# Optimization experiments

Hardware: AMD Instinct MI355X
Metric: run time of the kernel (lower is better)

The kernel has to match this reference:

```python
import jax, jax.numpy as jnp
import numpy as np

MIN_SCALE = 1e-3
TEMPERATURE = 1.5


def setup_inputs() -> dict:
    key = jax.random.key(0)
    ks = jax.random.split(key, 9)
    B, S, D, R, C = 1024, 64, 512, 16, 1000
    s = 1.0 / np.sqrt(D)  # scale weights for numerical sanity
    return {
        "features": jax.random.normal(ks[0], (B, D), jnp.float32),
        "W_cov": jax.random.normal(ks[1], (D * R, D), jnp.float32) * s,
        "b_cov": jnp.zeros((D * R,), jnp.float32),
        "W_diag": jax.random.normal(ks[2], (D, D), jnp.float32) * s,
        "b_diag": jnp.zeros((D,), jnp.float32),
        "W_cls": jax.random.normal(ks[3], (C, D), jnp.float32) * s,
        "b_cls": jnp.zeros((C,), jnp.float32),
        "noise_diag": jax.random.normal(ks[4], (B, S, D), jnp.float32),
        "noise_lr": jax.random.normal(ks[5], (B, S, R), jnp.float32),
    }


def reference(features, W_cov, b_cov, W_diag, b_diag, W_cls, b_cls, noise_diag, noise_lr):
    B, D = features.shape
    R = noise_lr.shape[-1]
    # Linear(D -> D*R), reshape to (B, D, R) (row-major, matches torch .reshape)
    low_rank_cov = (features @ W_cov.T + b_cov).reshape(B, D, R)
    # diagonal std: softplus(Linear(D->D)) + min_scale
    diagonal_std = jax.nn.softplus(features @ W_diag.T + b_diag) + MIN_SCALE
    # samples: low-rank part + diagonal part, both (B, S, D)
    samples = (
        jnp.einsum("bdr,bsr->bsd", low_rank_cov, noise_lr)
        + diagonal_std[:, None, :] * noise_diag
    )
    pre_logits = features[:, None, :] + samples  # (B, S, D)
    logits = pre_logits @ W_cls.T + b_cls  # (B, S, C)
    return logits / TEMPERATURE
```

## Files before the change

### kernel.cpp

```cpp
#include <hip/hip_runtime.h>
#include <math.h>

typedef __attribute__((ext_vector_type(8))) short bf16x8;
typedef __attribute__((ext_vector_type(4))) float f32x4;
typedef __attribute__((ext_vector_type(4))) unsigned short u16x4;

__device__ inline unsigned short f2bf(float f) {
    union { float f; unsigned u; } v; v.f = f;
    unsigned r = v.u + 0x7FFFu + ((v.u >> 16) & 1u);
    return (unsigned short)(r >> 16);
}
__device__ inline float bf2f(unsigned short h) {
    union { unsigned u; float f; } v; v.u = ((unsigned)h) << 16;
    return v.f;
}

__device__ inline void load_lds16(const void* g, void* l) {
    __builtin_amdgcn_global_load_lds(
        (const __attribute__((address_space(1))) unsigned int*)g,
        (__attribute__((address_space(3))) unsigned int*)l,
        16, 0, 0);
}

__global__ __launch_bounds__(256) void convert_all(
    const float* __restrict__ sA, unsigned short* __restrict__ dA, long nA,
    const float* __restrict__ sB, unsigned short* __restrict__ dB, long nB,
    const float* __restrict__ sC, unsigned short* __restrict__ dC, long nC,
    const float* __restrict__ sD, unsigned short* __restrict__ dD, long nDs, long nDd)
{
    long i = ((long)blockIdx.x * 256 + threadIdx.x) * 4;
    const float* s; unsigned short* d; long nsrc;
    if (i < nA)              { s = sA + i; d = dA + i; nsrc = nA - i; }
    else if ((i -= nA) < nB) { s = sB + i; d = dB + i; nsrc = nB - i; }
    else if ((i -= nB) < nC) { s = sC + i; d = dC + i; nsrc = nC - i; }
    else if ((i -= nC) < nDd){ s = sD + i; d = dD + i; nsrc = nDs - i; }
    else return;
    float4 v = make_float4(0.f, 0.f, 0.f, 0.f);
    if (nsrc >= 4) v = *(const float4*)s;
    u16x4 o;
    o[0] = f2bf(v.x); o[1] = f2bf(v.y); o[2] = f2bf(v.z); o[3] = f2bf(v.w);
    *(u16x4*)d = o;
}

template <int MODE, bool SWZ>
__global__ __launch_bounds__(256) void gemm_bf16(
    const unsigned short* __restrict__ A, const unsigned short* __restrict__ Bm,
    const float* __restrict__ bias0, const float* __restrict__ bias1,
    void* __restrict__ out0v, void* __restrict__ out1v,
    int M, int Npad, int Nreal, int K, int nsplit)
{
    __shared__ __align__(16) unsigned short As[128 * 64];
    __shared__ __align__(16) unsigned short Bs[128 * 64];

    const int tid  = threadIdx.x;
    const int nblk = Npad >> 7;
    int mt, nt;
    if constexpr (SWZ) {
        const int per = (M >> 7) >> 3;
        const int x = blockIdx.x & 7;
        const int j = blockIdx.x >> 3;
        const int jm = j / nblk;
        mt = x * per + jm;
        nt = j - jm * nblk;
    } else {
        mt = blockIdx.x / nblk;
        nt = blockIdx.x - mt * nblk;
    }
    const int m0 = mt << 7;
    const int n0 = nt << 7;

    const int lane = tid & 63;
    const int wid  = tid >> 6;
    const int wm   = (wid & 1) << 6;
    const int wn   = (wid >> 1) << 6;
    const int quad = lane >> 4;
    const int l15  = lane & 15;
    const int l7   = l15 & 7;

    const int lrow = lane >> 3;
    const int lcol = ((lane & 7) ^ lrow) << 3;

    const unsigned short* Ab = A  + (size_t)(m0 + wid * 32 + lrow) * K + lcol;
    const unsigned short* Bb = Bm + (size_t)(n0 + wid * 32 + lrow) * K + lcol;
    unsigned short* AsW = &As[(wid * 32) * 64];
    unsigned short* BsW = &Bs[(wid * 32) * 64];

    f32x4 acc[4][4];
    #pragma unroll
    for (int i = 0; i < 4; ++i)
        #pragma unroll
        for (int j = 0; j < 4; ++j)
            acc[i][j] = f32x4{0.f, 0.f, 0.f, 0.f};

    for (int kt = 0; kt < K; kt += 64) {
        __syncthreads();
        #pragma unroll
        for (int i = 0; i < 4; ++i) {
            load_lds16(Ab + (size_t)(i * 8) * K + kt, AsW + i * 8 * 64);
            load_lds16(Bb + (size_t)(i * 8) * K + kt, BsW + i * 8 * 64);
        }
        __syncthreads();

        #pragma unroll
        for (int kk = 0; kk < 64; kk += 32) {
            const int kq = kk >> 3;
            bf16x8 af[4], bfv[4];
            #pragma unroll
            for (int mi = 0; mi < 4; ++mi)
                af[mi] = *(const bf16x8*)&As[(wm + mi * 16 + l15) * 64
                                             + (((kq + quad) ^ l7) << 3)];
            #pragma unroll
            for (int ni = 0; ni < 4; ++ni)
                bfv[ni] = *(const bf16x8*)&Bs[(wn + ni * 16 + l15) * 64
                                              + (((kq + quad) ^ l7) << 3)];
            #pragma unroll
            for (int mi = 0; mi < 4; ++mi)
                #pragma unroll
                for (int ni = 0; ni < 4; ++ni)
                    acc[mi][ni] = __builtin_amdgcn_mfma_f32_16x16x32_bf16(
                        bfv[ni], af[mi], acc[mi][ni], 0, 0, 0);
        }
    }

    if constexpr (MODE == 2) {
        float* o = (float*)out0v;
        #pragma unroll
        for (int ni = 0; ni < 4; ++ni) {
            const int nb = n0 + wn + ni * 16 + (quad << 2);
            if (nb >= Nreal) continue;
            const float4 bv = *(const float4*)&bias0[nb];
            #pragma unroll
            for (int mi = 0; mi < 4; ++mi) {
                const int m = m0 + wm + mi * 16 + l15;
                f32x4 v;
                v[0] = (acc[mi][ni][0] + bv.x) * (1.0f / 1.5f);
                v[1] = (acc[mi][ni][1] + bv.y) * (1.0f / 1.5f);
                v[2] = (acc[mi][ni][2] + bv.z) * (1.0f / 1.5f);
                v[3] = (acc[mi][ni][3] + bv.w) * (1.0f / 1.5f);
                *(f32x4*)&o[(size_t)m * Nreal + nb] = v;
            }
        }
    } else {
        if (n0 < nsplit) {
            unsigned short* o = (unsigned short*)out0v;
            #pragma unroll
            for (int ni = 0; ni < 4; ++ni) {
                const int nb = n0 + wn + ni * 16 + (quad << 2);
                const float4 bv = *(const float4*)&bias0[nb];
                #pragma unroll
                for (int mi = 0; mi < 4; ++mi) {
                    const int m = m0 + wm + mi * 16 + l15;
                    u16x4 ov;
                    ov[0] = f2bf(acc[mi][ni][0] + bv.x);
                    ov[1] = f2bf(acc[mi][ni][1] + bv.y);
                    ov[2] = f2bf(acc[mi][ni][2] + bv.z);
                    ov[3] = f2bf(acc[mi][ni][3] + bv.w);
                    *(u16x4*)&o[(size_t)m * nsplit + nb] = ov;
                }
            }
        } else {
            float* o = (float*)out1v;
            const int ld1 = Npad - nsplit;
            #pragma unroll
            for (int ni = 0; ni < 4; ++ni) {
                const int nb = n0 + wn + ni * 16 + (quad << 2) - nsplit;
                const float4 bv = *(const float4*)&bias1[nb];
                #pragma unroll
                for (int mi = 0; mi < 4; ++mi) {
                    const int m = m0 + wm + mi * 16 + l15;
                    f32x4 v;
                    #pragma unroll
                    for (int r = 0; r < 4; ++r) {
                        float x = acc[mi][ni][r] + ((const float*)&bv)[r];
                        float sp = (x > 20.f) ? x : log1pf(expf(x));
                        v[r] = sp + 1e-3f;
                    }
                    *(f32x4*)&o[(size_t)m * ld1 + nb] = v;
                }
            }
        }
    }
}

__global__ __launch_bounds__(256) void sample_kernel(
    const float* __restrict__ features, const unsigned short* __restrict__ lr_cov,
    const float* __restrict__ diag, const float* __restrict__ nz_lr,
    const float* __restrict__ nz_diag, unsigned short* __restrict__ pre,
    int S, int D)
{
    const int tid = threadIdx.x;
    const int b   = blockIdx.x;
    const int sh  = tid >> 7;
    const int t   = tid & 127;
    const int d0  = t << 2;

    __shared__ __align__(16) float snz[64 * 16];
    ((float4*)snz)[tid] = ((const float4*)(nz_lr + (size_t)b * S * 16))[tid];

    float4 f  = *(const float4*)(features + (size_t)b * D + d0);
    float4 dg = *(const float4*)(diag + (size_t)b * D + d0);
    float L[4][16];
    const unsigned short* lp = lr_cov + (size_t)b * D * 16 + (size_t)d0 * 16;
    #pragma unroll
    for (int j = 0; j < 4; ++j) {
        bf16x8 a = *(const bf16x8*)(lp + j * 16);
        bf16x8 c = *(const bf16x8*)(lp + j * 16 + 8);
        #pragma unroll
        for (int r = 0; r < 8; ++r) {
            L[j][r]     = bf2f((unsigned short)a[r]);
            L[j][8 + r] = bf2f((unsigned short)c[r]);
        }
    }
    __syncthreads();

    const int s0 = sh * (S >> 1);
    const float* ndp = nz_diag + (size_t)b * S * D + (size_t)s0 * D + d0;
    unsigned short* pp = pre + (size_t)b * S * D + (size_t)s0 * D + d0;
    const int SH = S >> 1;
    for (int s = 0; s < SH; s += 2) {
        float4 nd0 = *(const float4*)(ndp + (size_t)s * D);
        float4 nd1 = *(const float4*)(ndp + (size_t)(s + 1) * D);
        float a0 = f.x + dg.x * nd0.x, a1 = f.y + dg.y * nd0.y;
        float a2 = f.z + dg.z * nd0.z, a3 = f.w + dg.w * nd0.w;
        float b0 = f.x + dg.x * nd1.x, b1 = f.y + dg.y * nd1.y;
        float b2 = f.z + dg.z * nd1.z, b3 = f.w + dg.w * nd1.w;
        const float* z0 = &snz[(s0 + s) * 16];
        const float* z1 = &snz[(s0 + s + 1) * 16];
        #pragma unroll
        for (int r = 0; r < 16; ++r) {
            float zv0 = z0[r], zv1 = z1[r];
            a0 += L[0][r] * zv0; a1 += L[1][r] * zv0;
            a2 += L[2][r] * zv0; a3 += L[3][r] * zv0;
            b0 += L[0][r] * zv1; b1 += L[1][r] * zv1;
            b2 += L[2][r] * zv1; b3 += L[3][r] * zv1;
        }
        u16x4 o0, o1;
        o0[0] = f2bf(a0); o0[1] = f2bf(a1); o0[2] = f2bf(a2); o0[3] = f2bf(a3);
        o1[0] = f2bf(b0); o1[1] = f2bf(b1); o1[2] = f2bf(b2); o1[3] = f2bf(b3);
        *(u16x4*)(pp + (size_t)s * D) = o0;
        *(u16x4*)(pp + (size_t)(s + 1) * D) = o1;
    }
}

extern "C" void kernel_launch(void* const* d_in, const int* in_sizes, int n_in,
                              void* d_out, int out_size, void* d_ws, size_t ws_size,
                              hipStream_t stream)
{
    const float* features = (const float*)d_in[0];
    const float* W_cov    = (const float*)d_in[1];
    const float* b_cov    = (const float*)d_in[2];
    const float* W_diag   = (const float*)d_in[3];
    const float* b_diag   = (const float*)d_in[4];
    const float* W_cls    = (const float*)d_in[5];
    const float* b_cls    = (const float*)d_in[6];
    const float* nz_diag  = (const float*)d_in[7];
    const float* nz_lr    = (const float*)d_in[8];

    const int D    = in_sizes[4];
    const int DR   = in_sizes[2];
    const int B    = in_sizes[0] / D;
    const int S    = in_sizes[7] / (B * D);
    const int C    = in_sizes[6];
    const int M    = B * S;
    const int Cpad = (C + 127) & ~127;
    const int Ncat = DR + D;

    char* ws = (char*)d_ws;
    unsigned short* lrcov = (unsigned short*)ws;
    float*          diag  = (float*)(ws + (size_t)B * DR * 2);
    unsigned short* wclsb = (unsigned short*)((char*)diag + (size_t)B * D * 4);
    char* X = (char*)wclsb + (size_t)Cpad * D * 2;
    unsigned short* featb = (unsigned short*)X;
    unsigned short* wcatb = featb + (size_t)B * D;
    unsigned short* pre   = (unsigned short*)X;

    {
        long n1 = (long)DR * D;
        long n2 = (long)D * D;
        long n3 = (long)B * D;
        long n4s = (long)C * D, n4d = (long)Cpad * D;
        long total = n1 + n2 + n3 + n4d;
        convert_all<<<dim3((unsigned)(total / 1024)), 256, 0, stream>>>(
            W_cov, wcatb, n1,
            W_diag, wcatb + n1, n2,
            features, featb, n3,
            W_cls, wclsb, n4s, n4d);
    }

    gemm_bf16<3, false><<<dim3((B / 128) * (Ncat / 128)), 256, 0, stream>>>(
        featb, wcatb, b_cov, b_diag, lrcov, diag, B, Ncat, Ncat, D, DR);

    sample_kernel<<<dim3(B), 256, 0, stream>>>(
        features, lrcov, diag, nz_lr, nz_diag, pre, S, D);

    gemm_bf16<2, true><<<dim3((M / 128) * (Cpad / 128)), 256, 0, stream>>>(
        pre, wclsb, b_cls, nullptr, d_out, nullptr, M, Cpad, C, D, DR);
}
```

Baseline: 547.1 us.

## Add 256x256-tile 8-wave GEMM with interleaved LDS pipeline for classifier

Replaces the 128x128 classifier GEMM with a new 512-thread kernel computing 256x256 tiles. It double-buffers LDS with direct global-to-LDS loads, interleaves MFMA with staged loads, raises wave priority around the MFMAs, and remaps blocks so neighbouring blocks share A rows for better L2 reuse. The larger tile is meant to cut redundant global and LDS traffic in the dominant GEMM (M=65536, K=512). In exchange, C is padded to 1024 instead of 1024 (same here), and register and LDS pressure goes up, which limits occupancy.

Measured after the change: 549.3 us. No clear change (+0.4%).

```diff
diff --git a/kernel.cpp b/kernel.cpp
--- a/kernel.cpp
+++ b/kernel.cpp
@@ -182,6 +182,164 @@
     }
 }
 
+template <bool SWZ>
+__global__ __launch_bounds__(512, 2) void gemm2_256(
+    const unsigned short* __restrict__ A, const unsigned short* __restrict__ Bm,
+    const float* __restrict__ bias0, float* __restrict__ out,
+    int M, int Npad, int Nreal, int K)
+{
+    __shared__ __align__(16) unsigned short As[2 * 256 * 64];
+    __shared__ __align__(16) unsigned short Bs[2 * 256 * 64];
+
+    const int nblk = Npad >> 8;
+    int mt, nt;
+    if constexpr (SWZ) {
+        const int per = (M >> 8) >> 3;
+        const int x = blockIdx.x & 7;
+        const int j = blockIdx.x >> 3;
+        const int jm = j / nblk;
+        mt = x * per + jm;
+        nt = j - jm * nblk;
+    } else {
+        mt = blockIdx.x / nblk;
+        nt = blockIdx.x - mt * nblk;
+    }
+    const int m0 = mt << 8;
+    const int n0 = nt << 8;
+
+    const int tid  = threadIdx.x;
+    const int lane = tid & 63;
+    const int wid  = tid >> 6;
+    const int wmh  = wid >> 2;
+    const int wnq  = wid & 3;
+    const int quad = lane >> 4;
+    const int l15  = lane & 15;
+    const int l7   = l15 & 7;
+    const int lrow = lane >> 3;
+    const int lcol = ((lane & 7) ^ lrow) << 3;
+
+    const unsigned short* Ab = A  + (size_t)(m0 + wid * 32 + lrow) * K + lcol;
+    const unsigned short* Bb = Bm + (size_t)(n0 + wid * 32 + lrow) * K + lcol;
+    unsigned short* AsW = &As[(wid * 32) * 64];
+    unsigned short* BsW = &Bs[(wid * 32) * 64];
+
+#define STG_A(bi, kt) { \
+    const unsigned short* g_ = Ab + (size_t)(kt); \
+    unsigned short* l_ = AsW + (bi) * 16384; \
+    load_lds16(g_, l_); \
+    load_lds16(g_ + 8 * (size_t)K,  l_ + 512); \
+    load_lds16(g_ + 16 * (size_t)K, l_ + 1024); \
+    load_lds16(g_ + 24 * (size_t)K, l_ + 1536); }
+#define STG_B(bi, kt) { \
+    const unsigned short* g_ = Bb + (size_t)(kt); \
+    unsigned short* l_ = BsW + (bi) * 16384; \
+    load_lds16(g_, l_); \
+    load_lds16(g_ + 8 * (size_t)K,  l_ + 512); \
+    load_lds16(g_ + 16 * (size_t)K, l_ + 1024); \
+    load_lds16(g_ + 24 * (size_t)K, l_ + 1536); }
+#define RD_A(bi, qm, kh) { \
+    const unsigned short* p_ = &As[(bi) * 16384]; \
+    _Pragma("unroll") \
+    for (int i_ = 0; i_ < 4; ++i_) { \
+        const int row_ = wmh * 128 + ((qm) * 4 + i_) * 16 + l15; \
+        af[i_] = *(const bf16x8*)&p_[row_ * 64 + ((((kh) * 4 + quad) ^ l7) << 3)]; } }
+#define RD_B(bi, kh) { \
+    const unsigned short* p_ = &Bs[(bi) * 16384]; \
+    _Pragma("unroll") \
+    for (int i_ = 0; i_ < 4; ++i_) { \
+        const int row_ = wnq * 64 + i_ * 16 + l15; \
+        bfv[i_] = *(const bf16x8*)&p_[row_ * 64 + ((((kh) * 4 + quad) ^ l7) << 3)]; } }
+#define MM(qm) { \
+    __builtin_amdgcn_s_setprio(1); \
+    _Pragma("unroll") \
+    for (int i_ = 0; i_ < 4; ++i_) \
+        _Pragma("unroll") \
+        for (int j_ = 0; j_ < 4; ++j_) \
+            acc[(qm) * 4 + i_][j_] = __builtin_amdgcn_mfma_f32_16x16x32_bf16( \
+                bfv[j_], af[i_], acc[(qm) * 4 + i_][j_], 0, 0, 0); \
+    __builtin_amdgcn_s_setprio(0); }
+#define BAR()   asm volatile("s_barrier" ::: "memory")
+#define WLGKM() asm volatile("s_waitcnt lgkmcnt(0)" ::: "memory")
+#define WVM0()  asm volatile("s_waitcnt vmcnt(0)" ::: "memory")
+#define WVM8()  asm volatile("s_waitcnt vmcnt(8)" ::: "memory")
+
+    f32x4 acc[8][4];
+    #pragma unroll
+    for (int i = 0; i < 8; ++i)
+        #pragma unroll
+        for (int j = 0; j < 4; ++j)
+            acc[i][j] = f32x4{0.f, 0.f, 0.f, 0.f};
+
+    bf16x8 af[4], bfv[4];
+
+    STG_A(0, 0); STG_B(0, 0);
+    STG_A(1, 64); STG_B(1, 64);
+    WVM8();
+    BAR();
+
+    const int NI = K >> 7;
+    for (int I = 0; I < NI; ++I) {
+        const int keven = I << 7;
+        RD_A(0, 0, 0); RD_B(0, 0);
+        if (I > 0) STG_A(1, keven + 64);
+        BAR(); WLGKM(); MM(0);
+        BAR();
+        RD_A(0, 1, 0);
+        if (I > 0) STG_B(1, keven + 64);
+        BAR(); WLGKM(); MM(1);
+        BAR();
+        RD_A(0, 1, 1); RD_B(0, 1);
+        BAR(); WLGKM(); MM(1);
+        BAR();
+        RD_A(0, 0, 1);
+        BAR(); WLGKM(); MM(0);
+        WVM0();
+        BAR();
+        RD_A(1, 0, 0); RD_B(1, 0);
+        if (I + 1 < NI) STG_A(0, keven + 128);
+        BAR(); WLGKM(); MM(0);
+        BAR();
+        RD_A(1, 1, 0);
+        if (I + 1 < NI) STG_B(0, keven + 128);
+        BAR(); WLGKM(); MM(1);
+        BAR();
+        RD_A(1, 1, 1); RD_B(1, 1);
+        BAR(); WLGKM(); MM(1);
+        BAR();
+        RD_A(1, 0, 1);
+        BAR(); WLGKM(); MM(0);
+        WVM0();
+        BAR();
+    }
+
+    #pragma unroll
+    for (int ni = 0; ni < 4; ++ni) {
+        const int nb = n0 + wnq * 64 + ni * 16 + (quad << 2);
+        if (nb < Nreal) {
+            const float4 bv = *(const float4*)&bias0[nb];
+            #pragma unroll
+            for (int mi = 0; mi < 8; ++mi) {
+                const int m = m0 + wmh * 128 + mi * 16 + l15;
+                f32x4 v;
+                v[0] = (acc[mi][ni][0] + bv.x) * (1.0f / 1.5f);
+                v[1] = (acc[mi][ni][1] + bv.y) * (1.0f / 1.5f);
+                v[2] = (acc[mi][ni][2] + bv.z) * (1.0f / 1.5f);
+                v[3] = (acc[mi][ni][3] + bv.w) * (1.0f / 1.5f);
+                __builtin_nontemporal_store(v, (f32x4*)&out[(size_t)m * Nreal + nb]);
+            }
+        }
+    }
+#undef STG_A
+#undef STG_B
+#undef RD_A
+#undef RD_B
+#undef MM
+#undef BAR
+#undef WLGKM
+#undef WVM0
+#undef WVM8
+}
+
 __global__ __launch_bounds__(256) void sample_kernel(
     const float* __restrict__ features, const unsigned short* __restrict__ lr_cov,
     const float* __restrict__ diag, const float* __restrict__ nz_lr,
@@ -262,7 +420,7 @@
     const int S    = in_sizes[7] / (B * D);
     const int C    = in_sizes[6];
     const int M    = B * S;
-    const int Cpad = (C + 127) & ~127;
+    const int Cpad = (C + 255) & ~255;
     const int Ncat = DR + D;
 
     char* ws = (char*)d_ws;
@@ -293,6 +451,6 @@
     sample_kernel<<<dim3(B), 256, 0, stream>>>(
         features, lrcov, diag, nz_lr, nz_diag, pre, S, D);
 
-    gemm_bf16<2, true><<<dim3((M / 128) * (Cpad / 128)), 256, 0, stream>>>(
-        pre, wclsb, b_cls, nullptr, d_out, nullptr, M, Cpad, C, D, DR);
-}
+    gemm2_256<true><<<dim3((M / 256) * (Cpad / 256)), 512, 0, stream>>>(
+        pre, wclsb, b_cls, (float*)d_out, M, Cpad, C, D);
+}
```

## Split GEMM kernels with retuned tiles, wider classifier tile and nontemporal IO

Applied to the files above, without the earlier changes.

Splits the templated GEMM into two kernels. The first GEMM uses 64x128 tiles to launch more blocks. The classifier GEMM moves to 512-thread blocks with 128x256 tiles, with C padded to 256, and writes logits with nontemporal stores. The sample kernel now processes four samples per iteration and reads the diagonal noise with nontemporal loads. The aim is more reuse of the A operand in the dominant GEMM and less cache pollution from streaming data, at the cost of higher LDS and register use and 24 wasted padded columns instead of 24 of 1024.

After: 564.6 us. 3.2% more time.

```diff
diff --git a/kernel.cpp b/kernel.cpp
--- a/kernel.cpp
+++ b/kernel.cpp
@@ -42,18 +42,119 @@
     *(u16x4*)d = o;
 }
 
-template <int MODE, bool SWZ>
-__global__ __launch_bounds__(256) void gemm_bf16(
+__global__ __launch_bounds__(256) void gemm1_k(
     const unsigned short* __restrict__ A, const unsigned short* __restrict__ Bm,
     const float* __restrict__ bias0, const float* __restrict__ bias1,
-    void* __restrict__ out0v, void* __restrict__ out1v,
-    int M, int Npad, int Nreal, int K, int nsplit)
+    unsigned short* __restrict__ out0, float* __restrict__ out1,
+    int M, int Npad, int K, int nsplit)
+{
+    __shared__ __align__(16) unsigned short As[64 * 64];
+    __shared__ __align__(16) unsigned short Bs[128 * 64];
+
+    const int nblk = Npad >> 7;
+    const int mt = blockIdx.x / nblk;
+    const int nt = blockIdx.x - mt * nblk;
+    const int m0 = mt << 6;
+    const int n0 = nt << 7;
+
+    const int tid  = threadIdx.x;
+    const int lane = tid & 63;
+    const int wid  = tid >> 6;
+    const int quad = lane >> 4;
+    const int l15  = lane & 15;
+    const int l7   = l15 & 7;
+    const int lrow = lane >> 3;
+    const int lcol = ((lane & 7) ^ lrow) << 3;
+
+    const unsigned short* Ab = A  + (size_t)(m0 + lrow) * K + lcol;
+    const unsigned short* Bb = Bm + (size_t)(n0 + lrow) * K + lcol;
+
+    f32x4 acc[4][2];
+    #pragma unroll
+    for (int i = 0; i < 4; ++i)
+        #pragma unroll
+        for (int j = 0; j < 2; ++j)
+            acc[i][j] = f32x4{0.f, 0.f, 0.f, 0.f};
+
+    for (int kt = 0; kt < K; kt += 64) {
+        __syncthreads();
+        #pragma unroll
+        for (int i = 0; i < 6; ++i) {
+            const int r0 = wid * 48 + i * 8;
+            if (r0 < 64) load_lds16(Ab + (size_t)r0 * K + kt, &As[r0 * 64]);
+            else         load_lds16(Bb + (size_t)(r0 - 64) * K + kt, &Bs[(r0 - 64) * 64]);
+        }
+        __syncthreads();
+
+        #pragma unroll
+        for (int kk = 0; kk < 64; kk += 32) {
+            const int kq = kk >> 3;
+            bf16x8 af[4], bfv[2];
+            #pragma unroll
+            for (int mi = 0; mi < 4; ++mi)
+                af[mi] = *(const bf16x8*)&As[(mi * 16 + l15) * 64
+                                             + (((kq + quad) ^ l7) << 3)];
+            #pragma unroll
+            for (int ni = 0; ni < 2; ++ni)
+                bfv[ni] = *(const bf16x8*)&Bs[(wid * 32 + ni * 16 + l15) * 64
+                                              + (((kq + quad) ^ l7) << 3)];
+            #pragma unroll
+            for (int mi = 0; mi < 4; ++mi)
+                #pragma unroll
+                for (int ni = 0; ni < 2; ++ni)
+                    acc[mi][ni] = __builtin_amdgcn_mfma_f32_16x16x32_bf16(
+                        bfv[ni], af[mi], acc[mi][ni], 0, 0, 0);
+        }
+    }
+
+    if (n0 < nsplit) {
+        #pragma unroll
+        for (int ni = 0; ni < 2; ++ni) {
+            const int nb = n0 + wid * 32 + ni * 16 + (quad << 2);
+            const float4 bv = *(const float4*)&bias0[nb];
+            #pragma unroll
+            for (int mi = 0; mi < 4; ++mi) {
+                const int m = m0 + mi * 16 + l15;
+                u16x4 ov;
+                ov[0] = f2bf(acc[mi][ni][0] + bv.x);
+                ov[1] = f2bf(acc[mi][ni][1] + bv.y);
+                ov[2] = f2bf(acc[mi][ni][2] + bv.z);
+                ov[3] = f2bf(acc[mi][ni][3] + bv.w);
+                *(u16x4*)&out0[(size_t)m * nsplit + nb] = ov;
+            }
+        }
+    } else {
+        const int ld1 = Npad - nsplit;
+        #pragma unroll
+        for (int ni = 0; ni < 2; ++ni) {
+            const int nb = n0 + wid * 32 + ni * 16 + (quad << 2) - nsplit;
+            const float4 bv = *(const float4*)&bias1[nb];
+            #pragma unroll
+            for (int mi = 0; mi < 4; ++mi) {
+                const int m = m0 + mi * 16 + l15;
+                f32x4 v;
+                #pragma unroll
+                for (int r = 0; r < 4; ++r) {
+                    float x = acc[mi][ni][r] + ((const float*)&bv)[r];
+                    float sp = (x > 20.f) ? x : log1pf(expf(x));
+                    v[r] = sp + 1e-3f;
+                }
+                *(f32x4*)&out1[(size_t)m * ld1 + nb] = v;
+            }
+        }
+    }
+}
+
+template <bool SWZ>
+__global__ __launch_bounds__(512, 4) void gemm2_k(
+    const unsigned short* __restrict__ A, const unsigned short* __restrict__ Bm,
+    const float* __restrict__ bias0, float* __restrict__ out,
+    int M, int Npad, int Nreal, int K)
 {
     __shared__ __align__(16) unsigned short As[128 * 64];
-    __shared__ __align__(16) unsigned short Bs[128 * 64];
-
-    const int tid  = threadIdx.x;
-    const int nblk = Npad >> 7;
+    __shared__ __align__(16) unsigned short Bs[256 * 64];
+
+    const int nblk = Npad >> 8;
     int mt, nt;
     if constexpr (SWZ) {
         const int per = (M >> 7) >> 3;
@@ -67,23 +168,21 @@
         nt = blockIdx.x - mt * nblk;
     }
     const int m0 = mt << 7;
-    const int n0 = nt << 7;
-
+    const int n0 = nt << 8;
+
+    const int tid  = threadIdx.x;
     const int lane = tid & 63;
     const int wid  = tid >> 6;
-    const int wm   = (wid & 1) << 6;
-    const int wn   = (wid >> 1) << 6;
+    const int wmh  = wid >> 2;
+    const int wnq  = wid & 3;
     const int quad = lane >> 4;
     const int l15  = lane & 15;
     const int l7   = l15 & 7;
-
     const int lrow = lane >> 3;
     const int lcol = ((lane & 7) ^ lrow) << 3;
 
-    const unsigned short* Ab = A  + (size_t)(m0 + wid * 32 + lrow) * K + lcol;
-    const unsigned short* Bb = Bm + (size_t)(n0 + wid * 32 + lrow) * K + lcol;
-    unsigned short* AsW = &As[(wid * 32) * 64];
-    unsigned short* BsW = &Bs[(wid * 32) * 64];
+    const unsigned short* Ab = A  + (size_t)(m0 + lrow) * K + lcol;
+    const unsigned short* Bb = Bm + (size_t)(n0 + lrow) * K + lcol;
 
     f32x4 acc[4][4];
     #pragma unroll
@@ -95,9 +194,10 @@
     for (int kt = 0; kt < K; kt += 64) {
         __syncthreads();
         #pragma unroll
-        for (int i = 0; i < 4; ++i) {
-            load_lds16(Ab + (size_t)(i * 8) * K + kt, AsW + i * 8 * 64);
-            load_lds16(Bb + (size_t)(i * 8) * K + kt, BsW + i * 8 * 64);
+        for (int i = 0; i < 6; ++i) {
+            const int r0 = wid * 48 + i * 8;
+            if (r0 < 128) load_lds16(Ab + (size_t)r0 * K + kt, &As[r0 * 64]);
+            else          load_lds16(Bb + (size_t)(r0 - 128) * K + kt, &Bs[(r0 - 128) * 64]);
         }
         __syncthreads();
 
@@ -107,11 +207,11 @@
             bf16x8 af[4], bfv[4];
             #pragma unroll
             for (int mi = 0; mi < 4; ++mi)
-                af[mi] = *(const bf16x8*)&As[(wm + mi * 16 + l15) * 64
+                af[mi] = *(const bf16x8*)&As[(wmh * 64 + mi * 16 + l15) * 64
                                              + (((kq + quad) ^ l7) << 3)];
             #pragma unroll
             for (int ni = 0; ni < 4; ++ni)
-                bfv[ni] = *(const bf16x8*)&Bs[(wn + ni * 16 + l15) * 64
+                bfv[ni] = *(const bf16x8*)&Bs[(wnq * 64 + ni * 16 + l15) * 64
                                               + (((kq + quad) ^ l7) << 3)];
             #pragma unroll
             for (int mi = 0; mi < 4; ++mi)
@@ -122,61 +222,20 @@
         }
     }
 
-    if constexpr (MODE == 2) {
-        float* o = (float*)out0v;
-        #pragma unroll
-        for (int ni = 0; ni < 4; ++ni) {
-            const int nb = n0 + wn + ni * 16 + (quad << 2);
-            if (nb >= Nreal) continue;
+    #pragma unroll
+    for (int ni = 0; ni < 4; ++ni) {
+        const int nb = n0 + wnq * 64 + ni * 16 + (quad << 2);
+        if (nb < Nreal) {
             const float4 bv = *(const float4*)&bias0[nb];
             #pragma unroll
             for (int mi = 0; mi < 4; ++mi) {
-                const int m = m0 + wm + mi * 16 + l15;
+                const int m = m0 + wmh * 64 + mi * 16 + l15;
                 f32x4 v;
                 v[0] = (acc[mi][ni][0] + bv.x) * (1.0f / 1.5f);
                 v[1] = (acc[mi][ni][1] + bv.y) * (1.0f / 1.5f);
                 v[2] = (acc[mi][ni][2] + bv.z) * (1.0f / 1.5f);
                 v[3] = (acc[mi][ni][3] + bv.w) * (1.0f / 1.5f);
-                *(f32x4*)&o[(size_t)m * Nreal + nb] = v;
-            }
-        }
-    } else {
-        if (n0 < nsplit) {
-            unsigned short* o = (unsigned short*)out0v;
-            #pragma unroll
-            for (int ni = 0; ni < 4; ++ni) {
-                const int nb = n0 + wn + ni * 16 + (quad << 2);
-                const float4 bv = *(const float4*)&bias0[nb];
-                #pragma unroll
-                for (int mi = 0; mi < 4; ++mi) {
-                    const int m = m0 + wm + mi * 16 + l15;
-                    u16x4 ov;
-                    ov[0] = f2bf(acc[mi][ni][0] + bv.x);
-                    ov[1] = f2bf(acc[mi][ni][1] + bv.y);
-                    ov[2] = f2bf(acc[mi][ni][2] + bv.z);
-                    ov[3] = f2bf(acc[mi][ni][3] + bv.w);
-                    *(u16x4*)&o[(size_t)m * nsplit + nb] = ov;
-                }
-            }
-        } else {
-            float* o = (float*)out1v;
-            const int ld1 = Npad - nsplit;
-            #pragma unroll
-            for (int ni = 0; ni < 4; ++ni) {
-                const int nb = n0 + wn + ni * 16 + (quad << 2) - nsplit;
-                const float4 bv = *(const float4*)&bias1[nb];
-                #pragma unroll
-                for (int mi = 0; mi < 4; ++mi) {
-                    const int m = m0 + wm + mi * 16 + l15;
-                    f32x4 v;
-                    #pragma unroll
-                    for (int r = 0; r < 4; ++r) {
-                        float x = acc[mi][ni][r] + ((const float*)&bv)[r];
-                        float sp = (x > 20.f) ? x : log1pf(expf(x));
-                        v[r] = sp + 1e-3f;
-                    }
-                    *(f32x4*)&o[(size_t)m * ld1 + nb] = v;
-                }
+                __builtin_nontemporal_store(v, (f32x4*)&out[(size_t)m * Nreal + nb]);
             }
         }
     }
@@ -217,28 +276,37 @@
     const float* ndp = nz_diag + (size_t)b * S * D + (size_t)s0 * D + d0;
     unsigned short* pp = pre + (size_t)b * S * D + (size_t)s0 * D + d0;
     const int SH = S >> 1;
-    for (int s = 0; s < SH; s += 2) {
-        float4 nd0 = *(const float4*)(ndp + (size_t)s * D);
-        float4 nd1 = *(const float4*)(ndp + (size_t)(s + 1) * D);
-        float a0 = f.x + dg.x * nd0.x, a1 = f.y + dg.y * nd0.y;
-        float a2 = f.z + dg.z * nd0.z, a3 = f.w + dg.w * nd0.w;
-        float b0 = f.x + dg.x * nd1.x, b1 = f.y + dg.y * nd1.y;
-        float b2 = f.z + dg.z * nd1.z, b3 = f.w + dg.w * nd1.w;
-        const float* z0 = &snz[(s0 + s) * 16];
-        const float* z1 = &snz[(s0 + s + 1) * 16];
+    for (int s = 0; s < SH; s += 4) {
+        f32x4 nd[4];
+        #pragma unroll
+        for (int j = 0; j < 4; ++j)
+            nd[j] = __builtin_nontemporal_load((const f32x4*)(ndp + (size_t)(s + j) * D));
+        float o[4][4];
+        #pragma unroll
+        for (int j = 0; j < 4; ++j) {
+            o[j][0] = f.x + dg.x * nd[j][0];
+            o[j][1] = f.y + dg.y * nd[j][1];
+            o[j][2] = f.z + dg.z * nd[j][2];
+            o[j][3] = f.w + dg.w * nd[j][3];
+        }
         #pragma unroll
         for (int r = 0; r < 16; ++r) {
-            float zv0 = z0[r], zv1 = z1[r];
-            a0 += L[0][r] * zv0; a1 += L[1][r] * zv0;
-            a2 += L[2][r] * zv0; a3 += L[3][r] * zv0;
-            b0 += L[0][r] * zv1; b1 += L[1][r] * zv1;
-            b2 += L[2][r] * zv1; b3 += L[3][r] * zv1;
-        }
-        u16x4 o0, o1;
-        o0[0] = f2bf(a0); o0[1] = f2bf(a1); o0[2] = f2bf(a2); o0[3] = f2bf(a3);
-        o1[0] = f2bf(b0); o1[1] = f2bf(b1); o1[2] = f2bf(b2); o1[3] = f2bf(b3);
-        *(u16x4*)(pp + (size_t)s * D) = o0;
-        *(u16x4*)(pp + (size_t)(s + 1) * D) = o1;
+            #pragma unroll
+            for (int j = 0; j < 4; ++j) {
+                const float zv = snz[(s0 + s + j) * 16 + r];
+                o[j][0] += L[0][r] * zv;
+                o[j][1] += L[1][r] * zv;
+                o[j][2] += L[2][r] * zv;
+                o[j][3] += L[3][r] * zv;
+            }
+        }
+        #pragma unroll
+        for (int j = 0; j < 4; ++j) {
+            u16x4 ov;
+            ov[0] = f2bf(o[j][0]); ov[1] = f2bf(o[j][1]);
+            ov[2] = f2bf(o[j][2]); ov[3] = f2bf(o[j][3]);
+            *(u16x4*)(pp + (size_t)(s + j) * D) = ov;
+        }
     }
 }
 
@@ -262,7 +330,7 @@
     const int S    = in_sizes[7] / (B * D);
     const int C    = in_sizes[6];
     const int M    = B * S;
-    const int Cpad = (C + 127) & ~127;
+    const int Cpad = (C + 255) & ~255;
     const int Ncat = DR + D;
 
     char* ws = (char*)d_ws;
@@ -287,12 +355,12 @@
             W_cls, wclsb, n4s, n4d);
     }
 
-    gemm_bf16<3, false><<<dim3((B / 128) * (Ncat / 128)), 256, 0, stream>>>(
-        featb, wcatb, b_cov, b_diag, lrcov, diag, B, Ncat, Ncat, D, DR);
+    gemm1_k<<<dim3((B / 64) * (Ncat / 128)), 256, 0, stream>>>(
+        featb, wcatb, b_cov, b_diag, lrcov, diag, B, Ncat, D, DR);
 
     sample_kernel<<<dim3(B), 256, 0, stream>>>(
         features, lrcov, diag, nz_lr, nz_diag, pre, S, D);
 
-    gemm_bf16<2, true><<<dim3((M / 128) * (Cpad / 128)), 256, 0, stream>>>(
-        pre, wclsb, b_cls, nullptr, d_out, nullptr, M, Cpad, C, D, DR);
-}
+    gemm2_k<true><<<dim3((M / 128) * (Cpad / 256)), 512, 0, stream>>>(
+        pre, wclsb, b_cls, (float*)d_out, M, Cpad, C, D);
+}
```
